# Kernel tuning notes

Hardware: AMD Instinct MI355X
Metric: run time of the kernel (lower is better)

## Reference

```python
import jax, jax.numpy as jnp
import numpy as np

EPS = 1e-5


def _bn(x, g, b):
    # training-mode BatchNorm2d over (N, H, W), biased variance
    m = jnp.mean(x, axis=(0, 2, 3), keepdims=True)
    v = jnp.var(x, axis=(0, 2, 3), keepdims=True)
    return (x - m) * jax.lax.rsqrt(v + EPS) * g[None, :, None, None] + b[None, :, None, None]


def _conv1x1(x, w):
    # x: [B, Cin, H, W], w: [Cout, Cin]
    return jnp.einsum('bchw,oc->bohw', x, w)


def _prop_attention(x, wq, wkv, wo, bo, obj_dict, bg_dict, rand_inds):
    B, C, H, W = x.shape  # B == 1
    heads, crop = rand_inds.shape[0], rand_inds.shape[1]
    dh = C // heads
    HW = H * W
    num_obj = crop // 2
    # original does x.clone().detach() before attention
    xd = jax.lax.stop_gradient(x)
    xh = xd.reshape(heads, dh, HW)  # batch=1 folded away (matches t.view(-1, crop**2))
    # pos[h, i, j] = flat pixel index gathered for head h, group i, slot j
    pos = jnp.concatenate(
        [obj_dict[rand_inds[:, :num_obj]], bg_dict[rand_inds[:, num_obj:]]], axis=1
    )  # [heads, crop, crop]
    tokens = jax.vmap(lambda xv, pv: xv[:, pv])(xh, pos)  # [heads, dh, crop, crop]
    tokens = tokens.transpose(0, 2, 3, 1).reshape(heads * crop, crop, dh)
    q = tokens @ wq.T
    k, v = jnp.split(tokens @ wkv.T, 2, axis=-1)
    dots = jnp.einsum('bie,bje->bij', q, k) * (dh ** -0.5)
    attn = jax.nn.softmax(dots, axis=-1)
    out = jnp.einsum('bij,bje->bie', attn, v)  # [heads*crop, crop, dh]
    # faithful to torch out.view(heads*crop, -1, crop): a raw row-major reinterpret
    out_r = out.reshape(heads, crop, dh, crop)
    vals = out_r.transpose(0, 2, 1, 3).reshape(heads, dh, crop * crop)
    pos_flat = pos.reshape(heads, crop * crop)
    # pos is a bijection onto [0, HW) per head -> invert and gather
    ar = jnp.arange(HW, dtype=jnp.int32)
    inv = jax.vmap(lambda p: jnp.zeros((HW,), jnp.int32).at[p].set(ar))(pos_flat)
    img = jax.vmap(lambda vh, ih: vh[:, ih])(vals, inv)  # [heads, dh, HW]
    img = img.reshape(1, heads * dh, H, W)
    # to_out: Linear(dim, dim) applied channels-last
    return jnp.einsum('bchw,oc->bohw', img, wo) + bo[None, :, None, None]


def setup_inputs():
    H = W = 300
    HW = H * W
    heads, crop = 2, H
    num_obj = crop // 2
    ch, emb = 256, 64
    dh = emb // heads
    key = jax.random.key(0)
    ks = jax.random.split(key, 10)
    x = jax.random.normal(ks[0], (1, ch, H, W), jnp.float32)
    perm = jax.random.permutation(ks[1], HW)
    obj_dict = perm[: HW // 2]
    bg_dict = perm[HW // 2 :]
    ri = []
    for h in range(heads):
        po = jax.random.permutation(jax.random.fold_in(ks[2], h), HW // 2).reshape(num_obj, crop)
        pb = jax.random.permutation(jax.random.fold_in(ks[3], h), HW // 2).reshape(crop - num_obj, crop)
        ri.append(jnp.concatenate([po, pb], axis=0))
    rand_inds = jnp.stack(ri)  # [heads, crop, crop]
    w_conv1 = jax.random.normal(ks[4], (emb, ch), jnp.float32) / np.sqrt(ch)
    wq = jax.random.normal(ks[5], (dh, dh), jnp.float32) / np.sqrt(dh)
    wkv = jax.random.normal(ks[6], (2 * dh, dh), jnp.float32) / np.sqrt(dh)
    wo = jax.random.normal(ks[7], (emb, emb), jnp.float32) / np.sqrt(emb)
    bo = jnp.zeros((emb,), jnp.float32)
    w_conv2 = jax.random.normal(ks[8], (emb, 2 * emb), jnp.float32) / np.sqrt(2 * emb)
    return {
        'x': x,
        'w_conv1': w_conv1,
        'bn1_g': jnp.ones((emb,), jnp.float32),
        'bn1_b': jnp.zeros((emb,), jnp.float32),
        'wq': wq,
        'wkv': wkv,
        'wo': wo,
        'bo': bo,
        'w_conv2': w_conv2,
        'bn2_g': jnp.ones((emb,), jnp.float32),
        'bn2_b': jnp.zeros((emb,), jnp.float32),
        'obj_dict': obj_dict,
        'bg_dict': bg_dict,
        'rand_inds': rand_inds,
    }


def reference(x, w_conv1, bn1_g, bn1_b, wq, wkv, wo, bo, w_conv2, bn2_g, bn2_b, obj_dict, bg_dict, rand_inds):
    x1 = jax.nn.relu(_bn(_conv1x1(x, w_conv1), bn1_g, bn1_b))
    xa = jax.nn.relu(_prop_attention(x1, wq, wkv, wo, bo, obj_dict, bg_dict, rand_inds))
    xc = jnp.concatenate([xa, x1], axis=1)
    return jax.nn.relu(_bn(_conv1x1(xc, w_conv2), bn2_g, bn2_b))
```

## Files before the change

kernel.cpp:

```cpp
#include <hip/hip_runtime.h>
#include <hip/hip_bf16.h>

#define HW 90000
#define CROP 300
#define C2EXP 0.25503492f

typedef __attribute__((ext_vector_type(8))) short s8v;
typedef __attribute__((ext_vector_type(4))) float f4v;
#define MFMA16(a,b,c) __builtin_amdgcn_mfma_f32_16x16x32_bf16(a,b,c,0,0,0)

__device__ __forceinline__ unsigned short f2bf(float f) {
    unsigned int u = __float_as_uint(f);
    return (unsigned short)((u + 0x7fffu + ((u >> 16) & 1u)) >> 16);
}
__device__ __forceinline__ float bf2f(unsigned short s) {
    return __uint_as_float(((unsigned int)s) << 16);
}
__device__ __forceinline__ unsigned pk_trunc(float a, float b) {
    return __builtin_amdgcn_perm(__float_as_uint(b), __float_as_uint(a), 0x07060302u);
}
__device__ __forceinline__ unsigned pk_rne(float a, float b) {
    return (unsigned)f2bf(a) | ((unsigned)f2bf(b) << 16);
}
__device__ __forceinline__ s8v pack8(float4 u0, float4 u1) {
    s8v A;
    A[0] = (short)f2bf(u0.x); A[1] = (short)f2bf(u0.y);
    A[2] = (short)f2bf(u0.z); A[3] = (short)f2bf(u0.w);
    A[4] = (short)f2bf(u1.x); A[5] = (short)f2bf(u1.y);
    A[6] = (short)f2bf(u1.z); A[7] = (short)f2bf(u1.w);
    return A;
}

__global__ void prep_kernel(const float* __restrict__ w1, const float* __restrict__ wq,
                            const float* __restrict__ wkv, const float* __restrict__ wo,
                            const float* __restrict__ w2,
                            short* __restrict__ w1b, short* __restrict__ wqb,
                            short* __restrict__ wkvb, short* __restrict__ wob,
                            short* __restrict__ w2b) {
    int idx = blockIdx.x * blockDim.x + threadIdx.x;
    int stride = gridDim.x * blockDim.x;
    for (int i = idx; i < 16384; i += stride) w1b[i] = (short)f2bf(w1[i]);
    for (int i = idx; i < 1024; i += stride)  wqb[i] = (short)f2bf(wq[i]);
    for (int i = idx; i < 2048; i += stride)  wkvb[i] = (short)f2bf(wkv[i]);
    for (int i = idx; i < 4096; i += stride)  wob[i] = (short)f2bf(wo[i]);
    for (int i = idx; i < 8192; i += stride)  w2b[i] = (short)f2bf(w2[i]);
}

__global__ __launch_bounds__(256, 2) void conv1_mfma(const float* __restrict__ x,
        const short* __restrict__ w1b, short* __restrict__ y1b, float* __restrict__ stat) {
    __shared__ __align__(16) short lw[16384];
    __shared__ float red[2][4][64];
    const int wave = threadIdx.x >> 6, lane = threadIdx.x & 63;
    const int q = lane >> 4, n = lane & 15;
    for (int i = threadIdx.x; i < 2048; i += 256)
        ((uint4*)lw)[i] = ((const uint4*)w1b)[i];
    __syncthreads();

    const int s0 = blockIdx.x * 256 + wave * 64;
    const int pb = (s0 + 4 * n <= HW - 4) ? (s0 + 4 * n) : (HW - 4);
    f4v acc[4][4];
#pragma unroll
    for (int mt = 0; mt < 4; ++mt)
#pragma unroll
        for (int nt = 0; nt < 4; ++nt) acc[mt][nt] = f4v{0.f, 0.f, 0.f, 0.f};

    float4 cur[8], nxt[8];
#pragma unroll
    for (int j = 0; j < 8; ++j)
        cur[j] = *(const float4*)(x + (size_t)(q * 8 + j) * HW + pb);
#pragma unroll
    for (int kb = 0; kb < 8; ++kb) {
        if (kb < 7) {
#pragma unroll
            for (int j = 0; j < 8; ++j)
                nxt[j] = *(const float4*)(x + (size_t)((kb + 1) * 32 + q * 8 + j) * HW + pb);
        }
        s8v A[4];
#pragma unroll
        for (int mt = 0; mt < 4; ++mt) {
            union { unsigned u[4]; s8v v; } am;
#pragma unroll
            for (int w = 0; w < 4; ++w)
                am.u[w] = pk_trunc(((const float*)&cur[2 * w])[mt],
                                   ((const float*)&cur[2 * w + 1])[mt]);
            A[mt] = am.v;
        }
#pragma unroll
        for (int mt = 0; mt < 4; ++mt)
#pragma unroll
            for (int nt = 0; nt < 4; ++nt) {
                int c = (nt & 1) + 2 * n + 32 * (nt >> 1);
                s8v B = *(const s8v*)(lw + c * 256 + kb * 32 + q * 8);
                acc[mt][nt] = MFMA16(A[mt], B, acc[mt][nt]);
            }
        if (kb < 7) {
#pragma unroll
            for (int j = 0; j < 8; ++j) cur[j] = nxt[j];
        }
    }

    float s1[4] = {0.f, 0.f, 0.f, 0.f}, s2[4] = {0.f, 0.f, 0.f, 0.f};
#pragma unroll
    for (int mt = 0; mt < 4; ++mt)
#pragma unroll
        for (int r = 0; r < 4; ++r) {
            int p = s0 + 4 * (q * 4 + r) + mt;
            if (p < HW) {
                float v0 = acc[mt][0][r], v1 = acc[mt][1][r];
                float v2 = acc[mt][2][r], v3 = acc[mt][3][r];
                *(unsigned*)(y1b + (size_t)p * 64 + 2 * n)      = pk_rne(v0, v1);
                *(unsigned*)(y1b + (size_t)p * 64 + 32 + 2 * n) = pk_rne(v2, v3);
                s1[0] += v0; s2[0] += v0 * v0;
                s1[1] += v1; s2[1] += v1 * v1;
                s1[2] += v2; s2[2] += v2 * v2;
                s1[3] += v3; s2[3] += v3 * v3;
            }
        }
#pragma unroll
    for (int m = 16; m < 64; m <<= 1)
#pragma unroll
        for (int nt = 0; nt < 4; ++nt) {
            s1[nt] += __shfl_xor(s1[nt], m, 64);
            s2[nt] += __shfl_xor(s2[nt], m, 64);
        }
    if (lane < 16)
#pragma unroll
        for (int nt = 0; nt < 4; ++nt) {
            int c = (nt & 1) + 2 * lane + 32 * (nt >> 1);
            red[0][wave][c] = s1[nt];
            red[1][wave][c] = s2[nt];
        }
    __syncthreads();
    if (threadIdx.x < 128) {
        int k = threadIdx.x >> 6, c = threadIdx.x & 63;
        atomicAdd(&stat[k * 64 + c],
                  red[k][0][c] + red[k][1][c] + red[k][2][c] + red[k][3][c]);
    }
}

__global__ void bn_fin_kernel(const float* __restrict__ stat,
        const float* __restrict__ g, const float* __restrict__ b, float* __restrict__ ab) {
    int c = threadIdx.x;
    float m = stat[c] * (1.f / HW);
    float v = stat[64 + c] * (1.f / HW) - m * m;
    float ac = g[c] * rsqrtf(v + 1e-5f);
    ab[c] = ac;
    ab[64 + c] = b[c] - m * ac;
}

__global__ __launch_bounds__(256) void bnrelu_kernel(const short* __restrict__ y1b,
        const float* __restrict__ ab1, short* __restrict__ x1b) {
    int t = blockIdx.x * 256 + threadIdx.x;
    if (t >= 720000) return;
    int cb = 8 * (t & 7);
    float4 a0 = *(const float4*)(ab1 + cb), a1 = *(const float4*)(ab1 + cb + 4);
    float4 b0 = *(const float4*)(ab1 + 64 + cb), b1 = *(const float4*)(ab1 + 64 + cb + 4);
    uint4 u = ((const uint4*)y1b)[t];
    float r0 = fmaxf(fmaf(a0.x, __uint_as_float(u.x << 16), b0.x), 0.f);
    float r1 = fmaxf(fmaf(a0.y, __uint_as_float(u.x & 0xffff0000u), b0.y), 0.f);
    float r2 = fmaxf(fmaf(a0.z, __uint_as_float(u.y << 16), b0.z), 0.f);
    float r3 = fmaxf(fmaf(a0.w, __uint_as_float(u.y & 0xffff0000u), b0.w), 0.f);
    float r4 = fmaxf(fmaf(a1.x, __uint_as_float(u.z << 16), b1.x), 0.f);
    float r5 = fmaxf(fmaf(a1.y, __uint_as_float(u.z & 0xffff0000u), b1.y), 0.f);
    float r6 = fmaxf(fmaf(a1.z, __uint_as_float(u.w << 16), b1.z), 0.f);
    float r7 = fmaxf(fmaf(a1.w, __uint_as_float(u.w & 0xffff0000u), b1.w), 0.f);
    uint4 o;
    o.x = pk_rne(r0, r1); o.y = pk_rne(r2, r3);
    o.z = pk_rne(r4, r5); o.w = pk_rne(r6, r7);
    ((uint4*)x1b)[t] = o;
}

__global__ __launch_bounds__(512, 4) void attn_mfma_kernel(const short* __restrict__ x1b,
        const short* __restrict__ wqb, const short* __restrict__ wkvb,
        const int* __restrict__ obj, const int* __restrict__ bg,
        const int* __restrict__ rinds, short* __restrict__ imgb) {
    __shared__ __align__(16) short tokQ[304 * 40];
    __shared__ __align__(16) short kbuf[304 * 40];
    __shared__ __align__(16) short vt[32 * 328];
    __shared__ __align__(16) short pbuf[8 * 16 * 40];
    __shared__ int possh[304];
    const int b = blockIdx.x;
    const int h = b / CROP, i = b - h * CROP;
    const int tid = threadIdx.x;
    const int wave = tid >> 6, lane = tid & 63, q = lane >> 4, n = lane & 15;

    if (tid < 300) {
        int ri = rinds[h * HW + i * CROP + tid];
        possh[tid] = (i < 150) ? obj[ri] : bg[ri];
    } else if (tid < 380) {
        ((unsigned int*)(tokQ + 300 * 40))[tid - 300] = 0;
    } else if (tid < 460) {
        ((unsigned int*)(kbuf + 300 * 40))[tid - 380] = 0;
    }
    for (int ii = tid; ii < 320; ii += 512) {
        int e = ii / 10, w = ii - 10 * e;
        ((unsigned int*)vt)[e * 164 + 150 + w] = 0;
    }
    __syncthreads();

    for (int idx = tid; idx < 1200; idx += 512) {
        int j = idx >> 2, part = idx & 3;
        *(uint4*)(tokQ + j * 40 + part * 8) =
            *(const uint4*)(x1b + (size_t)possh[j] * 64 + h * 32 + part * 8);
    }
    __syncthreads();

    {
        s8v bq0 = *(const s8v*)(wqb + n * 32 + q * 8);
        s8v bq1 = *(const s8v*)(wqb + (16 + n) * 32 + q * 8);
        s8v bk0 = *(const s8v*)(wkvb + n * 32 + q * 8);
        s8v bk1 = *(const s8v*)(wkvb + (16 + n) * 32 + q * 8);
        s8v bv0 = *(const s8v*)(wkvb + (32 + n) * 32 + q * 8);
        s8v bv1 = *(const s8v*)(wkvb + (48 + n) * 32 + q * 8);
        f4v zz = {0.f, 0.f, 0.f, 0.f};
#pragma unroll
        for (int ti = 0; ti < 3; ++ti) {
            int t = wave + ti * 8;
            if (t < 19) {
                s8v at = *(const s8v*)(tokQ + (16 * t + n) * 40 + q * 8);
                f4v qf0 = MFMA16(at, bq0, zz);
                f4v qf1 = MFMA16(at, bq1, zz);
                f4v kf0 = MFMA16(at, bk0, zz);
                f4v kf1 = MFMA16(at, bk1, zz);
                f4v vf0 = MFMA16(at, bv0, zz);
                f4v vf1 = MFMA16(at, bv1, zz);
#pragma unroll
                for (int r = 0; r < 4; ++r) {
                    int row = 16 * t + q * 4 + r;
                    tokQ[row * 40 + n]      = (short)f2bf(qf0[r]);
                    tokQ[row * 40 + 16 + n] = (short)f2bf(qf1[r]);
                    kbuf[row * 40 + n]      = (short)f2bf(kf0[r]);
                    kbuf[row * 40 + 16 + n] = (short)f2bf(kf1[r]);
                    vt[n * 328 + row]        = (short)f2bf(vf0[r]);
                    vt[(16 + n) * 328 + row] = (short)f2bf(vf1[r]);
                }
            }
        }
    }
    __syncthreads();

    s8v aQ[3];
#pragma unroll
    for (int ti = 0; ti < 3; ++ti) {
        int t = wave + ti * 8;
        aQ[ti] = (t < 19) ? *(const s8v*)(tokQ + (16 * t + n) * 40 + q * 8) : s8v{};
    }
    __syncthreads();

    f4v O[3][2];
    float lsum[3][4];
#pragma unroll
    for (int ti = 0; ti < 3; ++ti) {
        O[ti][0] = f4v{0.f, 0.f, 0.f, 0.f};
        O[ti][1] = f4v{0.f, 0.f, 0.f, 0.f};
#pragma unroll
        for (int r = 0; r < 4; ++r) lsum[ti][r] = 0.f;
    }
    short* pw = pbuf + wave * 16 * 40;
    f4v zz = {0.f, 0.f, 0.f, 0.f};
    for (int kb = 0; kb < 10; ++kb) {
        const int key0 = kb * 32 + n;
        const int key1 = kb * 32 + 16 + n;
        s8v bV0 = *(const s8v*)(vt + n * 328 + kb * 32 + q * 8);
        s8v bV1 = *(const s8v*)(vt + (16 + n) * 328 + kb * 32 + q * 8);
        s8v bK0 = *(const s8v*)(kbuf + key0 * 40 + q * 8);
        int r1 = key1 < 304 ? key1 : 303;
        s8v bK1 = *(const s8v*)(kbuf + r1 * 40 + q * 8);
#pragma unroll
        for (int ti = 0; ti < 3; ++ti) {
            int t = wave + ti * 8;
            if (t >= 19) continue;
            f4v s0 = MFMA16(aQ[ti], bK0, zz);
            f4v s1 = MFMA16(aQ[ti], bK1, zz);
#pragma unroll
            for (int r = 0; r < 4; ++r) {
                float e0 = (key0 < 300) ? exp2f(s0[r] * C2EXP) : 0.f;
                float e1 = (key1 < 300) ? exp2f(s1[r] * C2EXP) : 0.f;
                unsigned short p0 = f2bf(e0), p1 = f2bf(e1);
                lsum[ti][r] += bf2f(p0) + bf2f(p1);
                pw[(q * 4 + r) * 40 + n]      = (short)p0;
                pw[(q * 4 + r) * 40 + 16 + n] = (short)p1;
            }
            asm volatile("s_waitcnt lgkmcnt(0)" ::: "memory");
            s8v ap = *(const s8v*)(pw + n * 40 + q * 8);
            O[ti][0] = MFMA16(ap, bV0, O[ti][0]);
            O[ti][1] = MFMA16(ap, bV1, O[ti][1]);
        }
    }

#pragma unroll
    for (int m = 1; m < 16; m <<= 1) {
#pragma unroll
        for (int ti = 0; ti < 3; ++ti)
#pragma unroll
            for (int r = 0; r < 4; ++r)
                lsum[ti][r] += __shfl_xor(lsum[ti][r], m, 64);
    }
    short* outb = tokQ;
#pragma unroll
    for (int ti = 0; ti < 3; ++ti) {
        int t = wave + ti * 8;
        if (t >= 19) continue;
#pragma unroll
        for (int r = 0; r < 4; ++r) {
            float rl = 1.f / lsum[ti][r];
            int row = 16 * t + q * 4 + r;
            outb[row * 32 + n]      = (short)f2bf(O[ti][0][r] * rl);
            outb[row * 32 + 16 + n] = (short)f2bf(O[ti][1][r] * rl);
        }
    }
    __syncthreads();

    for (int idx = tid; idx < 9600; idx += 512) {
        int jj = idx >> 5, dd = idx & 31;
        imgb[(size_t)possh[jj] * 64 + h * 32 + dd] = outb[dd * CROP + jj];
    }
}

__global__ __launch_bounds__(256, 2) void fuse2_mfma(const short* __restrict__ imgb,
        const short* __restrict__ x1b,
        const short* __restrict__ wob, const short* __restrict__ w2b,
        const float* __restrict__ bo, float* __restrict__ y2, float* __restrict__ stat) {
    __shared__ __align__(16) short xas[4][16 * 72];
    __shared__ float ytr[64 * 133];
    __shared__ float red[2][4][64];
    const int wave = threadIdx.x >> 6, lane = threadIdx.x & 63;
    const int q = lane >> 4, n = lane & 15;
    s8v Bo[2][4], B2[4][4];
#pragma unroll
    for (int kb = 0; kb < 2; ++kb)
#pragma unroll
        for (int nt = 0; nt < 4; ++nt)
            Bo[kb][nt] = *(const s8v*)(wob + (nt * 16 + n) * 64 + kb * 32 + q * 8);
#pragma unroll
    for (int kb = 0; kb < 4; ++kb)
#pragma unroll
        for (int nt = 0; nt < 4; ++nt)
            B2[kb][nt] = *(const s8v*)(w2b + (nt * 16 + n) * 128 + kb * 32 + q * 8);
    float bov[4];
#pragma unroll
    for (int nt = 0; nt < 4; ++nt) bov[nt] = bo[nt * 16 + n];

    float s1[4] = {0.f, 0.f, 0.f, 0.f}, s2[4] = {0.f, 0.f, 0.f, 0.f};
    short* xw = xas[wave];
#pragma unroll
    for (int ti = 0; ti < 2; ++ti) {
        int tile = blockIdx.x * 8 + wave * 2 + ti;
        if (tile >= 5625) continue;
        int s0 = tile * 16;
        f4v xacc[4];
#pragma unroll
        for (int nt = 0; nt < 4; ++nt) xacc[nt] = f4v{0.f, 0.f, 0.f, 0.f};
#pragma unroll
        for (int kb = 0; kb < 2; ++kb) {
            s8v A = *(const s8v*)(imgb + (size_t)(s0 + n) * 64 + kb * 32 + q * 8);
#pragma unroll
            for (int nt = 0; nt < 4; ++nt) xacc[nt] = MFMA16(A, Bo[kb][nt], xacc[nt]);
        }
#pragma unroll
        for (int nt = 0; nt < 4; ++nt)
#pragma unroll
            for (int r = 0; r < 4; ++r) {
                float v = fmaxf(xacc[nt][r] + bov[nt], 0.f);
                xw[(q * 4 + r) * 72 + nt * 16 + n] = (short)f2bf(v);
            }
        asm volatile("s_waitcnt lgkmcnt(0)" ::: "memory");
        f4v yacc[4];
#pragma unroll
        for (int nt = 0; nt < 4; ++nt) yacc[nt] = f4v{0.f, 0.f, 0.f, 0.f};
#pragma unroll
        for (int kb = 0; kb < 2; ++kb) {
            s8v Axa = *(const s8v*)(xw + n * 72 + kb * 32 + q * 8);
#pragma unroll
            for (int nt = 0; nt < 4; ++nt) yacc[nt] = MFMA16(Axa, B2[kb][nt], yacc[nt]);
        }
#pragma unroll
        for (int kb = 0; kb < 2; ++kb) {
            s8v A = *(const s8v*)(x1b + (size_t)(s0 + n) * 64 + kb * 32 + q * 8);
#pragma unroll
            for (int nt = 0; nt < 4; ++nt) yacc[nt] = MFMA16(A, B2[kb + 2][nt], yacc[nt]);
        }
        int pl = wave * 32 + ti * 16;
#pragma unroll
        for (int nt = 0; nt < 4; ++nt)
#pragma unroll
            for (int r = 0; r < 4; ++r) {
                float v = yacc[nt][r];
                s1[nt] += v; s2[nt] += v * v;
                ytr[(nt * 16 + n) * 133 + pl + q * 4 + r] = v;
            }
    }
#pragma unroll
    for (int m = 16; m < 64; m <<= 1)
#pragma unroll
        for (int nt = 0; nt < 4; ++nt) {
            s1[nt] += __shfl_xor(s1[nt], m, 64);
            s2[nt] += __shfl_xor(s2[nt], m, 64);
        }
    if (lane < 16)
#pragma unroll
        for (int nt = 0; nt < 4; ++nt) {
            red[0][wave][nt * 16 + lane] = s1[nt];
            red[1][wave][nt * 16 + lane] = s2[nt];
        }
    __syncthreads();
    int s0b = blockIdx.x * 128;
    for (int i = threadIdx.x; i < 8192; i += 256) {
        int c = i >> 7, p = i & 127;
        int s = s0b + p;
        if (s < HW) y2[(size_t)c * HW + s] = ytr[c * 133 + p];
    }
    if (threadIdx.x < 128) {
        int k = threadIdx.x >> 6, c = threadIdx.x & 63;
        atomicAdd(&stat[k * 64 + c],
                  red[k][0][c] + red[k][1][c] + red[k][2][c] + red[k][3][c]);
    }
}

__global__ __launch_bounds__(256) void bn_out_kernel(const float* __restrict__ y2,
        const float* __restrict__ ab2, float* __restrict__ out) {
    int c = blockIdx.y;
    int s4 = blockIdx.x * 256 + threadIdx.x;
    if (s4 >= 22500) return;
    float a = ab2[c], b = ab2[64 + c];
    float4 v = *(const float4*)(y2 + (size_t)c * HW + s4 * 4);
    v.x = fmaxf(fmaf(a, v.x, b), 0.f);
    v.y = fmaxf(fmaf(a, v.y, b), 0.f);
    v.z = fmaxf(fmaf(a, v.z, b), 0.f);
    v.w = fmaxf(fmaf(a, v.w, b), 0.f);
    *(float4*)(out + (size_t)c * HW + s4 * 4) = v;
}

extern "C" void kernel_launch(void* const* d_in, const int* in_sizes, int n_in,
                              void* d_out, int out_size, void* d_ws, size_t ws_size,
                              hipStream_t stream) {
    const float* x   = (const float*)d_in[0];
    const float* w1  = (const float*)d_in[1];
    const float* g1  = (const float*)d_in[2];
    const float* b1  = (const float*)d_in[3];
    const float* wq  = (const float*)d_in[4];
    const float* wkv = (const float*)d_in[5];
    const float* wo  = (const float*)d_in[6];
    const float* bo  = (const float*)d_in[7];
    const float* w2  = (const float*)d_in[8];
    const float* g2  = (const float*)d_in[9];
    const float* b2  = (const float*)d_in[10];
    const int* obj   = (const int*)d_in[11];
    const int* bg    = (const int*)d_in[12];
    const int* rinds = (const int*)d_in[13];

    float* WSF  = (float*)d_ws;
    short* W1B  = (short*)d_ws;
    short* WOB  = W1B + 16384;
    short* W2B  = WOB + 4096;
    short* WQB  = W2B + 8192;
    short* WKVB = WQB + 1024;
    float* STAT = WSF + 16384;
    float* AB1  = STAT + 256;
    float* AB2  = AB1 + 128;
    short* Y1B  = (short*)(WSF + 16896);
    short* X1B  = Y1B + 5760000;
    short* IMGB = X1B + 5760000;
    float* Y2   = WSF + 16896 + 8640000;

    hipMemsetAsync(STAT, 0, 1024, stream);
    prep_kernel<<<16, 256, 0, stream>>>(w1, wq, wkv, wo, w2, W1B, WQB, WKVB, WOB, W2B);
    conv1_mfma<<<352, 256, 0, stream>>>(x, W1B, Y1B, STAT);
    bn_fin_kernel<<<1, 64, 0, stream>>>(STAT, g1, b1, AB1);
    bnrelu_kernel<<<2813, 256, 0, stream>>>(Y1B, AB1, X1B);
    attn_mfma_kernel<<<600, 512, 0, stream>>>(X1B, WQB, WKVB, obj, bg, rinds, IMGB);
    fuse2_mfma<<<704, 256, 0, stream>>>(IMGB, X1B, WOB, W2B, bo, Y2, STAT + 128);
    bn_fin_kernel<<<1, 64, 0, stream>>>(STAT + 128, g2, b2, AB2);
    bn_out_kernel<<<dim3(88, 64), 256, 0, stream>>>(Y2, AB2, (float*)d_out);
}
```

Measured before the change: 265.5 us.

## Fold Wq·Wk into one score matrix and shrink attention and conv1 blocks

Precomputes M = Wq^T·Wk scaled by the softmax exponent constant, so attention uses the raw tokens as keys and skips the separate K projection and its LDS buffer. The attention kernel drops to 384 threads with 4 row tiles per wave, stores V in a permuted layout, packs P by truncation, and special-cases the last key block. Conv1 halves pixels per block and doubles the grid for more occupancy. Precomputing the fused matrix in bf16 changes rounding, and the V column permutation must stay consistent with the P layout.

```diff
diff --git a/kernel.cpp b/kernel.cpp
--- a/kernel.cpp
+++ b/kernel.cpp
@@ -22,31 +22,28 @@
 __device__ __forceinline__ unsigned pk_rne(float a, float b) {
     return (unsigned)f2bf(a) | ((unsigned)f2bf(b) << 16);
 }
-__device__ __forceinline__ s8v pack8(float4 u0, float4 u1) {
-    s8v A;
-    A[0] = (short)f2bf(u0.x); A[1] = (short)f2bf(u0.y);
-    A[2] = (short)f2bf(u0.z); A[3] = (short)f2bf(u0.w);
-    A[4] = (short)f2bf(u1.x); A[5] = (short)f2bf(u1.y);
-    A[6] = (short)f2bf(u1.z); A[7] = (short)f2bf(u1.w);
-    return A;
-}
 
 __global__ void prep_kernel(const float* __restrict__ w1, const float* __restrict__ wq,
                             const float* __restrict__ wkv, const float* __restrict__ wo,
                             const float* __restrict__ w2,
-                            short* __restrict__ w1b, short* __restrict__ wqb,
-                            short* __restrict__ wkvb, short* __restrict__ wob,
-                            short* __restrict__ w2b) {
+                            short* __restrict__ w1b, short* __restrict__ wkvb,
+                            short* __restrict__ wob, short* __restrict__ w2b,
+                            short* __restrict__ msb) {
     int idx = blockIdx.x * blockDim.x + threadIdx.x;
     int stride = gridDim.x * blockDim.x;
     for (int i = idx; i < 16384; i += stride) w1b[i] = (short)f2bf(w1[i]);
-    for (int i = idx; i < 1024; i += stride)  wqb[i] = (short)f2bf(wq[i]);
     for (int i = idx; i < 2048; i += stride)  wkvb[i] = (short)f2bf(wkv[i]);
     for (int i = idx; i < 4096; i += stride)  wob[i] = (short)f2bf(wo[i]);
     for (int i = idx; i < 8192; i += stride)  w2b[i] = (short)f2bf(w2[i]);
-}
-
-__global__ __launch_bounds__(256, 2) void conv1_mfma(const float* __restrict__ x,
+    for (int i = idx; i < 1024; i += stride) {
+        int ep = i >> 5, e = i & 31;
+        float s = 0.f;
+        for (int a = 0; a < 32; ++a) s += wq[a * 32 + e] * wkv[a * 32 + ep];
+        msb[i] = (short)f2bf(s * C2EXP);
+    }
+}
+
+__global__ __launch_bounds__(256, 4) void conv1_mfma(const float* __restrict__ x,
         const short* __restrict__ w1b, short* __restrict__ y1b, float* __restrict__ stat) {
     __shared__ __align__(16) short lw[16384];
     __shared__ float red[2][4][64];
@@ -56,43 +53,43 @@
         ((uint4*)lw)[i] = ((const uint4*)w1b)[i];
     __syncthreads();
 
-    const int s0 = blockIdx.x * 256 + wave * 64;
-    const int pb = (s0 + 4 * n <= HW - 4) ? (s0 + 4 * n) : (HW - 4);
-    f4v acc[4][4];
-#pragma unroll
-    for (int mt = 0; mt < 4; ++mt)
+    const int s0 = blockIdx.x * 128 + wave * 32;
+    int pbx = s0 + 2 * n;
+    if (pbx > HW - 2) pbx = HW - 2;
+    f4v acc[2][4];
+#pragma unroll
+    for (int mt = 0; mt < 2; ++mt)
 #pragma unroll
         for (int nt = 0; nt < 4; ++nt) acc[mt][nt] = f4v{0.f, 0.f, 0.f, 0.f};
 
-    float4 cur[8], nxt[8];
+    float2 cur[8], nxt[8];
 #pragma unroll
     for (int j = 0; j < 8; ++j)
-        cur[j] = *(const float4*)(x + (size_t)(q * 8 + j) * HW + pb);
+        cur[j] = *(const float2*)(x + (size_t)(q * 8 + j) * HW + pbx);
 #pragma unroll
     for (int kb = 0; kb < 8; ++kb) {
         if (kb < 7) {
 #pragma unroll
             for (int j = 0; j < 8; ++j)
-                nxt[j] = *(const float4*)(x + (size_t)((kb + 1) * 32 + q * 8 + j) * HW + pb);
-        }
-        s8v A[4];
-#pragma unroll
-        for (int mt = 0; mt < 4; ++mt) {
-            union { unsigned u[4]; s8v v; } am;
-#pragma unroll
-            for (int w = 0; w < 4; ++w)
-                am.u[w] = pk_trunc(((const float*)&cur[2 * w])[mt],
-                                   ((const float*)&cur[2 * w + 1])[mt]);
-            A[mt] = am.v;
-        }
-#pragma unroll
-        for (int mt = 0; mt < 4; ++mt)
-#pragma unroll
-            for (int nt = 0; nt < 4; ++nt) {
-                int c = (nt & 1) + 2 * n + 32 * (nt >> 1);
-                s8v B = *(const s8v*)(lw + c * 256 + kb * 32 + q * 8);
-                acc[mt][nt] = MFMA16(A[mt], B, acc[mt][nt]);
-            }
+                nxt[j] = *(const float2*)(x + (size_t)((kb + 1) * 32 + q * 8 + j) * HW + pbx);
+        }
+        s8v A[2];
+        {
+            union { unsigned u[4]; s8v v; } a0, a1;
+#pragma unroll
+            for (int w = 0; w < 4; ++w) {
+                a0.u[w] = pk_trunc(cur[2 * w].x, cur[2 * w + 1].x);
+                a1.u[w] = pk_trunc(cur[2 * w].y, cur[2 * w + 1].y);
+            }
+            A[0] = a0.v; A[1] = a1.v;
+        }
+#pragma unroll
+        for (int nt = 0; nt < 4; ++nt) {
+            int c = (nt & 1) + 2 * n + 32 * (nt >> 1);
+            s8v B = *(const s8v*)(lw + c * 256 + kb * 32 + q * 8);
+            acc[0][nt] = MFMA16(A[0], B, acc[0][nt]);
+            acc[1][nt] = MFMA16(A[1], B, acc[1][nt]);
+        }
         if (kb < 7) {
 #pragma unroll
             for (int j = 0; j < 8; ++j) cur[j] = nxt[j];
@@ -101,10 +98,10 @@
 
     float s1[4] = {0.f, 0.f, 0.f, 0.f}, s2[4] = {0.f, 0.f, 0.f, 0.f};
 #pragma unroll
-    for (int mt = 0; mt < 4; ++mt)
+    for (int mt = 0; mt < 2; ++mt)
 #pragma unroll
         for (int r = 0; r < 4; ++r) {
-            int p = s0 + 4 * (q * 4 + r) + mt;
+            int p = s0 + 2 * (q * 4 + r) + mt;
             if (p < HW) {
                 float v0 = acc[mt][0][r], v1 = acc[mt][1][r];
                 float v2 = acc[mt][2][r], v3 = acc[mt][3][r];
@@ -170,15 +167,14 @@
     ((uint4*)x1b)[t] = o;
 }
 
-__global__ __launch_bounds__(512, 4) void attn_mfma_kernel(const short* __restrict__ x1b,
-        const short* __restrict__ wqb, const short* __restrict__ wkvb,
+__global__ __launch_bounds__(384, 4) void attn_mfma_kernel(const short* __restrict__ x1b,
+        const short* __restrict__ msb, const short* __restrict__ wkvb,
         const int* __restrict__ obj, const int* __restrict__ bg,
         const int* __restrict__ rinds, short* __restrict__ imgb) {
-    __shared__ __align__(16) short tokQ[304 * 40];
-    __shared__ __align__(16) short kbuf[304 * 40];
+    __shared__ __align__(16) short tok[304 * 40];
     __shared__ __align__(16) short vt[32 * 328];
-    __shared__ __align__(16) short pbuf[8 * 16 * 40];
-    __shared__ int possh[304];
+    __shared__ __align__(16) short pbuf[6 * 16 * 40];
+    __shared__ int possh[300];
     const int b = blockIdx.x;
     const int h = b / CROP, i = b - h * CROP;
     const int tid = threadIdx.x;
@@ -187,99 +183,96 @@
     if (tid < 300) {
         int ri = rinds[h * HW + i * CROP + tid];
         possh[tid] = (i < 150) ? obj[ri] : bg[ri];
-    } else if (tid < 380) {
-        ((unsigned int*)(tokQ + 300 * 40))[tid - 300] = 0;
-    } else if (tid < 460) {
-        ((unsigned int*)(kbuf + 300 * 40))[tid - 380] = 0;
-    }
-    for (int ii = tid; ii < 320; ii += 512) {
-        int e = ii / 10, w = ii - 10 * e;
-        ((unsigned int*)vt)[e * 164 + 150 + w] = 0;
-    }
-    __syncthreads();
-
-    for (int idx = tid; idx < 1200; idx += 512) {
+    }
+    for (int ii = tid; ii < 80; ii += 384)
+        ((unsigned*)(tok + 300 * 40))[ii] = 0;
+    for (int ii = tid; ii < 640; ii += 384) {
+        int e = ii / 20, w = ii - 20 * e;
+        ((unsigned*)vt)[e * 164 + 144 + w] = 0;
+    }
+    __syncthreads();
+
+    for (int idx = tid; idx < 1200; idx += 384) {
         int j = idx >> 2, part = idx & 3;
-        *(uint4*)(tokQ + j * 40 + part * 8) =
+        *(uint4*)(tok + j * 40 + part * 8) =
             *(const uint4*)(x1b + (size_t)possh[j] * 64 + h * 32 + part * 8);
     }
     __syncthreads();
 
+    short* pw = pbuf + wave * 16 * 40;
+    s8v aQ[4];
     {
-        s8v bq0 = *(const s8v*)(wqb + n * 32 + q * 8);
-        s8v bq1 = *(const s8v*)(wqb + (16 + n) * 32 + q * 8);
-        s8v bk0 = *(const s8v*)(wkvb + n * 32 + q * 8);
-        s8v bk1 = *(const s8v*)(wkvb + (16 + n) * 32 + q * 8);
+        s8v bq0 = *(const s8v*)(msb + n * 32 + q * 8);
+        s8v bq1 = *(const s8v*)(msb + (16 + n) * 32 + q * 8);
         s8v bv0 = *(const s8v*)(wkvb + (32 + n) * 32 + q * 8);
         s8v bv1 = *(const s8v*)(wkvb + (48 + n) * 32 + q * 8);
         f4v zz = {0.f, 0.f, 0.f, 0.f};
 #pragma unroll
-        for (int ti = 0; ti < 3; ++ti) {
-            int t = wave + ti * 8;
+        for (int ti = 0; ti < 4; ++ti) {
+            int t = wave + ti * 6;
+            aQ[ti] = s8v{};
             if (t < 19) {
-                s8v at = *(const s8v*)(tokQ + (16 * t + n) * 40 + q * 8);
+                s8v at = *(const s8v*)(tok + (16 * t + n) * 40 + q * 8);
                 f4v qf0 = MFMA16(at, bq0, zz);
                 f4v qf1 = MFMA16(at, bq1, zz);
-                f4v kf0 = MFMA16(at, bk0, zz);
-                f4v kf1 = MFMA16(at, bk1, zz);
                 f4v vf0 = MFMA16(at, bv0, zz);
                 f4v vf1 = MFMA16(at, bv1, zz);
 #pragma unroll
                 for (int r = 0; r < 4; ++r) {
                     int row = 16 * t + q * 4 + r;
-                    tokQ[row * 40 + n]      = (short)f2bf(qf0[r]);
-                    tokQ[row * 40 + 16 + n] = (short)f2bf(qf1[r]);
-                    kbuf[row * 40 + n]      = (short)f2bf(kf0[r]);
-                    kbuf[row * 40 + 16 + n] = (short)f2bf(kf1[r]);
-                    vt[n * 328 + row]        = (short)f2bf(vf0[r]);
-                    vt[(16 + n) * 328 + row] = (short)f2bf(vf1[r]);
+                    int phys = ((row >> 5) << 5) + 2 * (row & 15) + ((row >> 4) & 1);
+                    vt[n * 328 + phys]        = (short)f2bf(vf0[r]);
+                    vt[(16 + n) * 328 + phys] = (short)f2bf(vf1[r]);
+                    pw[(q * 4 + r) * 40 + n]      = (short)f2bf(qf0[r]);
+                    pw[(q * 4 + r) * 40 + 16 + n] = (short)f2bf(qf1[r]);
                 }
-            }
-        }
-    }
-    __syncthreads();
-
-    s8v aQ[3];
-#pragma unroll
-    for (int ti = 0; ti < 3; ++ti) {
-        int t = wave + ti * 8;
-        aQ[ti] = (t < 19) ? *(const s8v*)(tokQ + (16 * t + n) * 40 + q * 8) : s8v{};
-    }
-    __syncthreads();
-
-    f4v O[3][2];
-    float lsum[3][4];
-#pragma unroll
-    for (int ti = 0; ti < 3; ++ti) {
+                asm volatile("s_waitcnt lgkmcnt(0)" ::: "memory");
+                aQ[ti] = *(const s8v*)(pw + n * 40 + q * 8);
+            }
+        }
+    }
+    __syncthreads();
+
+    f4v O[4][2];
+    float lsum[4][4];
+#pragma unroll
+    for (int ti = 0; ti < 4; ++ti) {
         O[ti][0] = f4v{0.f, 0.f, 0.f, 0.f};
         O[ti][1] = f4v{0.f, 0.f, 0.f, 0.f};
 #pragma unroll
         for (int r = 0; r < 4; ++r) lsum[ti][r] = 0.f;
     }
-    short* pw = pbuf + wave * 16 * 40;
+    unsigned* pwd = (unsigned*)pw;
     f4v zz = {0.f, 0.f, 0.f, 0.f};
     for (int kb = 0; kb < 10; ++kb) {
-        const int key0 = kb * 32 + n;
-        const int key1 = kb * 32 + 16 + n;
+        s8v bK0 = *(const s8v*)(tok + (32 * kb + n) * 40 + q * 8);
+        s8v bK1 = (kb < 9) ? *(const s8v*)(tok + (32 * kb + 16 + n) * 40 + q * 8) : s8v{};
         s8v bV0 = *(const s8v*)(vt + n * 328 + kb * 32 + q * 8);
         s8v bV1 = *(const s8v*)(vt + (16 + n) * 328 + kb * 32 + q * 8);
-        s8v bK0 = *(const s8v*)(kbuf + key0 * 40 + q * 8);
-        int r1 = key1 < 304 ? key1 : 303;
-        s8v bK1 = *(const s8v*)(kbuf + r1 * 40 + q * 8);
-#pragma unroll
-        for (int ti = 0; ti < 3; ++ti) {
-            int t = wave + ti * 8;
+#pragma unroll
+        for (int ti = 0; ti < 4; ++ti) {
+            int t = wave + ti * 6;
             if (t >= 19) continue;
             f4v s0 = MFMA16(aQ[ti], bK0, zz);
-            f4v s1 = MFMA16(aQ[ti], bK1, zz);
-#pragma unroll
-            for (int r = 0; r < 4; ++r) {
-                float e0 = (key0 < 300) ? exp2f(s0[r] * C2EXP) : 0.f;
-                float e1 = (key1 < 300) ? exp2f(s1[r] * C2EXP) : 0.f;
-                unsigned short p0 = f2bf(e0), p1 = f2bf(e1);
-                lsum[ti][r] += bf2f(p0) + bf2f(p1);
-                pw[(q * 4 + r) * 40 + n]      = (short)p0;
-                pw[(q * 4 + r) * 40 + 16 + n] = (short)p1;
+            if (kb < 9) {
+                f4v s1 = MFMA16(aQ[ti], bK1, zz);
+#pragma unroll
+                for (int r = 0; r < 4; ++r) {
+                    float e0 = exp2f(s0[r]);
+                    float e1 = exp2f(s1[r]);
+                    unsigned pk = pk_trunc(e0, e1);
+                    lsum[ti][r] += __uint_as_float(pk << 16) +
+                                   __uint_as_float(pk & 0xffff0000u);
+                    pwd[(q * 4 + r) * 20 + n] = pk;
+                }
+            } else {
+#pragma unroll
+                for (int r = 0; r < 4; ++r) {
+                    float e0 = (n < 12) ? exp2f(s0[r]) : 0.f;
+                    unsigned pk = pk_trunc(e0, 0.f);
+                    lsum[ti][r] += __uint_as_float(pk << 16);
+                    pwd[(q * 4 + r) * 20 + n] = pk;
+                }
             }
             asm volatile("s_waitcnt lgkmcnt(0)" ::: "memory");
             s8v ap = *(const s8v*)(pw + n * 40 + q * 8);
@@ -287,19 +280,20 @@
             O[ti][1] = MFMA16(ap, bV1, O[ti][1]);
         }
     }
+    __syncthreads();
 
 #pragma unroll
     for (int m = 1; m < 16; m <<= 1) {
 #pragma unroll
-        for (int ti = 0; ti < 3; ++ti)
+        for (int ti = 0; ti < 4; ++ti)
 #pragma unroll
             for (int r = 0; r < 4; ++r)
                 lsum[ti][r] += __shfl_xor(lsum[ti][r], m, 64);
     }
-    short* outb = tokQ;
-#pragma unroll
-    for (int ti = 0; ti < 3; ++ti) {
-        int t = wave + ti * 8;
+    short* outb = tok;
+#pragma unroll
+    for (int ti = 0; ti < 4; ++ti) {
+        int t = wave + ti * 6;
         if (t >= 19) continue;
 #pragma unroll
         for (int r = 0; r < 4; ++r) {
@@ -311,7 +305,7 @@
     }
     __syncthreads();
 
-    for (int idx = tid; idx < 9600; idx += 512) {
+    for (int idx = tid; idx < 9600; idx += 384) {
         int jj = idx >> 5, dd = idx & 31;
         imgb[(size_t)possh[jj] * 64 + h * 32 + dd] = outb[dd * CROP + jj];
     }
@@ -453,8 +447,8 @@
     short* W1B  = (short*)d_ws;
     short* WOB  = W1B + 16384;
     short* W2B  = WOB + 4096;
-    short* WQB  = W2B + 8192;
-    short* WKVB = WQB + 1024;
+    short* WKVB = W2B + 8192;
+    short* MSB  = WKVB + 2048;
     float* STAT = WSF + 16384;
     float* AB1  = STAT + 256;
     float* AB2  = AB1 + 128;
@@ -464,11 +458,11 @@
     float* Y2   = WSF + 16896 + 8640000;
 
     hipMemsetAsync(STAT, 0, 1024, stream);
-    prep_kernel<<<16, 256, 0, stream>>>(w1, wq, wkv, wo, w2, W1B, WQB, WKVB, WOB, W2B);
-    conv1_mfma<<<352, 256, 0, stream>>>(x, W1B, Y1B, STAT);
+    prep_kernel<<<16, 256, 0, stream>>>(w1, wq, wkv, wo, w2, W1B, WKVB, WOB, W2B, MSB);
+    conv1_mfma<<<704, 256, 0, stream>>>(x, W1B, Y1B, STAT);
     bn_fin_kernel<<<1, 64, 0, stream>>>(STAT, g1, b1, AB1);
     bnrelu_kernel<<<2813, 256, 0, stream>>>(Y1B, AB1, X1B);
-    attn_mfma_kernel<<<600, 512, 0, stream>>>(X1B, WQB, WKVB, obj, bg, rinds, IMGB);
+    attn_mfma_kernel<<<600, 384, 0, stream>>>(X1B, MSB, WKVB, obj, bg, rinds, IMGB);
     fuse2_mfma<<<704, 256, 0, stream>>>(IMGB, X1B, WOB, W2B, bo, Y2, STAT + 128);
     bn_fin_kernel<<<1, 64, 0, stream>>>(STAT + 128, g2, b2, AB2);
     bn_out_kernel<<<dim3(88, 64), 256, 0, stream>>>(Y2, AB2, (float*)d_out);
```

Measured after the change: 271.5 us. 2.3% more time.
